# Performance work log

Measured on AMD Instinct MI355X. Metric: run time of the kernel, lower is better.

## Reference

```python
import jax, jax.numpy as jnp
import numpy as np
from jax import lax
from jax.scipy.special import logsumexp

B, T, K = 256, 1024, 64


def setup_inputs() -> dict:
    key = jax.random.key(0)
    k1, k2, k3 = jax.random.split(key, 3)
    y_true = jax.random.randint(k1, (B, T), 0, K)  # 0 == pad tag
    emissions = jax.random.normal(k2, (B, T, K), dtype=jnp.float32)
    transition = jax.random.normal(k3, (K, K), dtype=jnp.float32) * 0.1
    return {"y_true": y_true, "emissions": emissions, "transition": transition}


def _log_partition(emissions, mask, transition):
    # alpha_0 = emissions[:, 0, :] (TF code does not mask step 0)
    alpha0 = emissions[:, 0, :]  # [B, K]

    def step(alpha, xs):
        emit_t, m_t = xs  # [B, K], [B]
        # score[b, i, j] = alpha[b, i] + transition[i, j] + emit_t[b, j]
        score = alpha[:, :, None] + transition[None, :, :] + emit_t[:, None, :]
        new_a = logsumexp(score, axis=1)  # [B, K]
        new_a = jnp.where(m_t[:, None] > 0, new_a, alpha)
        return new_a, None

    xs = (jnp.swapaxes(emissions[:, 1:, :], 0, 1),  # [T-1, B, K]
          jnp.swapaxes(mask[:, 1:], 0, 1))           # [T-1, B]
    alpha, _ = lax.scan(step, alpha0, xs)
    return logsumexp(alpha, axis=1)  # [B]


def reference(y_true, emissions, transition):
    mask = (y_true != 0).astype(emissions.dtype)  # [B, T]
    yt = y_true.astype(jnp.int32)

    # emission scores of the gold path on masked emissions
    em_masked = emissions * mask[:, :, None]
    e_scores = jnp.take_along_axis(em_masked, yt[:, :, None], axis=2)[..., 0].sum(axis=1)  # [B]

    # transition scores of the gold path
    prev, nxt = yt[:, :-1], yt[:, 1:]
    t_scores = (transition[prev, nxt] * mask[:, 1:]).sum(axis=1)  # [B]

    log_z = _log_partition(emissions, mask, transition)  # [B]
    ll = e_scores + t_scores - log_z
    return -jnp.mean(ll)
```

## Files before the change

kernel.cpp:

```cpp
#include <hip/hip_runtime.h>

#define LOG2E 1.44269504088896340736f
#define LN2   0.69314718055994530942f

typedef short bf4 __attribute__((ext_vector_type(4)));
typedef float f4  __attribute__((ext_vector_type(4)));

static __device__ __forceinline__ unsigned short f2bf_rne(float f) {
    unsigned u = __float_as_uint(f);
    u += 0x7FFFu + ((u >> 16) & 1u);
    return (unsigned short)(u >> 16);
}
static __device__ __forceinline__ unsigned pack_bf_trunc(float lo, float hi) {
    return __builtin_amdgcn_perm(__float_as_uint(hi), __float_as_uint(lo), 0x07060302u);
}

static __device__ __forceinline__ f4 mfma16(bf4 a, bf4 b, f4 c) {
#if __has_builtin(__builtin_amdgcn_mfma_f32_16x16x16bf16_1k)
    return __builtin_amdgcn_mfma_f32_16x16x16bf16_1k(a, b, c, 0, 0, 0);
#else
    f4 d;
    asm("v_mfma_f32_16x16x16_bf16 %0, %1, %2, %3" : "=v"(d) : "v"(a), "v"(b), "v"(c));
    return d;
#endif
}
static __device__ __forceinline__ void mfma_fence() {
#if !__has_builtin(__builtin_amdgcn_mfma_f32_16x16x16bf16_1k)
    asm volatile("s_nop 7\ns_nop 7");
#endif
}

__global__ __attribute__((amdgpu_flat_work_group_size(64, 64), amdgpu_waves_per_eu(4)))
void crf_scan(const int* __restrict__ yg, const float* __restrict__ em,
              const float* __restrict__ tr, unsigned short* __restrict__ Pg)
{
    constexpr int T = 1024;
    const int c = blockIdx.x, b = blockIdx.y;
    const int lane = threadIdx.x, nl = lane & 15, q = lane >> 4;

    __shared__ __align__(16) float d_sh[64];

    bf4 afr[4][4];
    #pragma unroll
    for (int mt = 0; mt < 4; ++mt)
        #pragma unroll
        for (int kt = 0; kt < 4; ++kt) {
            bf4 v;
            #pragma unroll
            for (int j = 0; j < 4; ++j) {
                const int k = 16 * kt + 4 * q + j, m = 16 * mt + nl;
                v[j] = (short)f2bf_rne(exp2f(tr[k * 64 + m] * LOG2E));
            }
            afr[mt][kt] = v;
        }

    bf4 bfr[4][4];
    #pragma unroll
    for (int kt = 0; kt < 4; ++kt)
        #pragma unroll
        for (int nt = 0; nt < 4; ++nt) {
            bf4 v;
            #pragma unroll
            for (int j = 0; j < 4; ++j)
                v[j] = (short)((kt == nt && nl == 4 * q + j) ? 0x3F80 : 0);
            bfr[kt][nt] = v;
        }

    const int t0 = 1 + 64 * c;
    const int nsteps = (c == 15) ? 63 : 64;
    const float* emb = em + (size_t)b * T * 64;

    int tl = t0 + lane; if (tl > T - 1) tl = T - 1;
    const int yvl = yg[b * T + tl];
    const unsigned long long msk = __ballot(lane < nsteps && yvl != 0);

    float ldc = emb[t0 * 64 + lane];
    for (int s = 0; s < nsteps; ++s) {
        int tn = t0 + s + 1; if (tn > T - 1) tn = T - 1;
        const float ldn = emb[tn * 64 + lane];
        if ((msk >> s) & 1ull) {
            d_sh[lane] = exp2f(ldc * LOG2E - 7.0f);
            f4 dq[4];
            #pragma unroll
            for (int mt = 0; mt < 4; ++mt)
                dq[mt] = *(const f4*)&d_sh[16 * mt + 4 * q];
            #pragma unroll
            for (int nt = 0; nt < 4; ++nt) {
                f4 acc[4];
                #pragma unroll
                for (int mt = 0; mt < 4; ++mt) {
                    f4 a = mfma16(afr[mt][0], bfr[0][nt], (f4)(0.0f));
                    a = mfma16(afr[mt][1], bfr[1][nt], a);
                    a = mfma16(afr[mt][2], bfr[2][nt], a);
                    a = mfma16(afr[mt][3], bfr[3][nt], a);
                    acc[mt] = a;
                }
                mfma_fence();
                #pragma unroll
                for (int mt = 0; mt < 4; ++mt) {
                    union { uint2 u; bf4 v2; } wv;
                    wv.u.x = pack_bf_trunc(acc[mt][0] * dq[mt][0], acc[mt][1] * dq[mt][1]);
                    wv.u.y = pack_bf_trunc(acc[mt][2] * dq[mt][2], acc[mt][3] * dq[mt][3]);
                    bfr[mt][nt] = wv.v2;
                }
            }
        }
        ldc = ldn;
    }

    unsigned short* pg = Pg + ((size_t)(b * 16 + c) << 12);
    #pragma unroll
    for (int nt = 0; nt < 4; ++nt)
        #pragma unroll
        for (int kt = 0; kt < 4; ++kt)
            *(uint2*)(pg + (16 * nt + nl) * 64 + 16 * kt + 4 * q) =
                *(const uint2*)&bfr[kt][nt];
}

__global__ __attribute__((amdgpu_flat_work_group_size(256, 256)))
void crf_combine(const int* __restrict__ yg, const float* __restrict__ em,
                 const float* __restrict__ tr, const unsigned short* __restrict__ Pg,
                 float* __restrict__ out)
{
    constexpr int T = 1024;
    const int b = blockIdx.x, tid = threadIdx.x;
    const int w = tid >> 6, j = tid & 63;

    __shared__ __align__(16) float v_sh[64];
    __shared__ float red[3][4];

    float ep = 0.f, tp = 0.f; int cnt = 0;
    float v = 0.f, L = 0.f, vs = 0.f;

    if (w == 0) {
        const float e0 = em[(size_t)b * T * 64 + j];
        float M0 = e0;
        #pragma unroll
        for (int o = 32; o > 0; o >>= 1) M0 = fmaxf(M0, __shfl_xor(M0, o, 64));
        v = exp2f((e0 - M0) * LOG2E);
        L = M0;

        const unsigned short* row = Pg + ((size_t)(b * 16) << 12) + j * 64;
        uint4 pA[8], pB[8];
        #pragma unroll
        for (int r = 0; r < 8; ++r) pA[r] = *(const uint4*)(row + r * 8);

#define CHUNK_STEP(CUR, NXT, CIDX)                                                 \
        do {                                                                       \
            if ((CIDX) + 1 < 16) {      \
                const unsigned short* rn = row + ((size_t)((CIDX) + 1) << 12);     \
                _Pragma("unroll")                                                  \
                for (int r = 0; r < 8; ++r) NXT[r] = *(const uint4*)(rn + r * 8);  \
            }                                                                      \
            v_sh[j] = v;                             \
            float s0 = 0.f, s1 = 0.f, s2 = 0.f, s3 = 0.f;                          \
            _Pragma("unroll")                                                      \
            for (int r = 0; r < 8; ++r) {                                          \
                const uint4 qq = CUR[r];                                           \
                const float* vp = &v_sh[r * 8];                                    \
                s0 = fmaf(__uint_as_float(qq.x << 16),         vp[0], s0);         \
                s1 = fmaf(__uint_as_float(qq.x & 0xFFFF0000u), vp[1], s1);         \
                s2 = fmaf(__uint_as_float(qq.y << 16),         vp[2], s2);         \
                s3 = fmaf(__uint_as_float(qq.y & 0xFFFF0000u), vp[3], s3);         \
                s0 = fmaf(__uint_as_float(qq.z << 16),         vp[4], s0);         \
                s1 = fmaf(__uint_as_float(qq.z & 0xFFFF0000u), vp[5], s1);         \
                s2 = fmaf(__uint_as_float(qq.w << 16),         vp[6], s2);         \
                s3 = fmaf(__uint_as_float(qq.w & 0xFFFF0000u), vp[7], s3);         \
            }                                                                      \
            float s = (s0 + s1) + (s2 + s3);                                       \
            const unsigned sb =                                                    \
                (unsigned)__builtin_amdgcn_readlane((int)__float_as_uint(s), 0);   \
            const int ef = (int)((sb >> 23) & 0xFF);                               \
            if (ef > 0 && ef < 255 && ef != 127) {       \
                const int E = ef - 127;                                            \
                s *= __uint_as_float((unsigned)(127 - E) << 23);                   \
                L += (float)E * LN2;                                               \
            }                                                                      \
            v = s;                                                                 \
        } while (0)

        for (int cc = 0; cc < 16; cc += 2) {
            CHUNK_STEP(pA, pB, cc);
            CHUNK_STEP(pB, pA, cc + 1);
        }
#undef CHUNK_STEP

        vs = v;
        #pragma unroll
        for (int o = 32; o > 0; o >>= 1) vs += __shfl_xor(vs, o, 64);
    } else {
        const int* yb = yg + b * T;
        const int wt = tid - 64;
        for (int t = 1 + wt; t < T; t += 192) {
            const int yt = yb[t];
            if (yt != 0) {
                ++cnt;
                tp += tr[yb[t - 1] * 64 + yt];
                ep += em[((size_t)b * T + t) * 64 + yt];
            }
        }
        if (tid == 64) {
            const int y0 = yb[0];
            if (y0 != 0) ep += em[(size_t)b * T * 64 + y0];
        }
        #pragma unroll
        for (int o = 32; o > 0; o >>= 1) {
            ep  += __shfl_xor(ep, o, 64);
            tp  += __shfl_xor(tp, o, 64);
            cnt += __shfl_xor(cnt, o, 64);
        }
        if (j == 0) { red[0][w] = ep; red[1][w] = tp; red[2][w] = (float)cnt; }
    }
    __syncthreads();

    if (tid == 0) {
        const float eps = red[0][1] + red[0][2] + red[0][3];
        const float tps = red[1][1] + red[1][2] + red[1][3];
        const float cs  = red[2][1] + red[2][2] + red[2][3];
        const float logz = L + 7.0f * LN2 * cs + __log2f(vs) * LN2;
        atomicAdd(out, (eps + tps - logz) * (-1.0f / 256.0f));
    }
}

extern "C" void kernel_launch(void* const* d_in, const int* in_sizes, int n_in,
                              void* d_out, int out_size, void* d_ws, size_t ws_size,
                              hipStream_t stream) {
    const int*   y  = (const int*)d_in[0];
    const float* em = (const float*)d_in[1];
    const float* tr = (const float*)d_in[2];
    float* out = (float*)d_out;
    unsigned short* Pg = (unsigned short*)d_ws;

    hipMemsetAsync(out, 0, sizeof(float), stream);
    crf_scan<<<dim3(16, 256), dim3(64), 0, stream>>>(y, em, tr, Pg);
    crf_combine<<<dim3(256), dim3(256), 0, stream>>>(y, em, tr, Pg, out);
}
```

Baseline: 246.2 us.

## Interleave two independent chunk chains per wave in the CRF scan kernel

Each wavefront now processes two time chunks (c and c+8) of the same sequence, interleaving their MFMA chains so one chain's latency can hide behind the other. Masked steps are handled by a branchless select instead of skipping, so both chains always run the full MFMA work. The grid is halved and register pressure roughly doubles for the B-state fragments, which may reduce occupancy. The waves_per_eu hint is relaxed to allow that.

```diff
diff --git a/kernel.cpp b/kernel.cpp
--- a/kernel.cpp
+++ b/kernel.cpp
@@ -30,15 +30,15 @@
 #endif
 }
 
-__global__ __attribute__((amdgpu_flat_work_group_size(64, 64), amdgpu_waves_per_eu(4)))
+__global__ __attribute__((amdgpu_flat_work_group_size(64, 64), amdgpu_waves_per_eu(2, 4)))
 void crf_scan(const int* __restrict__ yg, const float* __restrict__ em,
               const float* __restrict__ tr, unsigned short* __restrict__ Pg)
 {
     constexpr int T = 1024;
-    const int c = blockIdx.x, b = blockIdx.y;
+    const int cA = blockIdx.x, b = blockIdx.y, cB = cA + 8;
     const int lane = threadIdx.x, nl = lane & 15, q = lane >> 4;
 
-    __shared__ __align__(16) float d_sh[64];
+    __shared__ __align__(16) float d_sh[2][64];
 
     bf4 afr[4][4];
     #pragma unroll
@@ -54,7 +54,7 @@
             afr[mt][kt] = v;
         }
 
-    bf4 bfr[4][4];
+    bf4 bfrA[4][4], bfrB[4][4];
     #pragma unroll
     for (int kt = 0; kt < 4; ++kt)
         #pragma unroll
@@ -63,58 +63,82 @@
             #pragma unroll
             for (int j = 0; j < 4; ++j)
                 v[j] = (short)((kt == nt && nl == 4 * q + j) ? 0x3F80 : 0);
-            bfr[kt][nt] = v;
-        }
-
-    const int t0 = 1 + 64 * c;
-    const int nsteps = (c == 15) ? 63 : 64;
+            bfrA[kt][nt] = v;
+            bfrB[kt][nt] = v;
+        }
+
     const float* emb = em + (size_t)b * T * 64;
-
-    int tl = t0 + lane; if (tl > T - 1) tl = T - 1;
-    const int yvl = yg[b * T + tl];
-    const unsigned long long msk = __ballot(lane < nsteps && yvl != 0);
-
-    float ldc = emb[t0 * 64 + lane];
-    for (int s = 0; s < nsteps; ++s) {
-        int tn = t0 + s + 1; if (tn > T - 1) tn = T - 1;
-        const float ldn = emb[tn * 64 + lane];
-        if ((msk >> s) & 1ull) {
-            d_sh[lane] = exp2f(ldc * LOG2E - 7.0f);
-            f4 dq[4];
-            #pragma unroll
-            for (int mt = 0; mt < 4; ++mt)
-                dq[mt] = *(const f4*)&d_sh[16 * mt + 4 * q];
-            #pragma unroll
-            for (int nt = 0; nt < 4; ++nt) {
-                f4 acc[4];
-                #pragma unroll
-                for (int mt = 0; mt < 4; ++mt) {
-                    f4 a = mfma16(afr[mt][0], bfr[0][nt], (f4)(0.0f));
-                    a = mfma16(afr[mt][1], bfr[1][nt], a);
-                    a = mfma16(afr[mt][2], bfr[2][nt], a);
-                    a = mfma16(afr[mt][3], bfr[3][nt], a);
-                    acc[mt] = a;
-                }
-                mfma_fence();
-                #pragma unroll
-                for (int mt = 0; mt < 4; ++mt) {
-                    union { uint2 u; bf4 v2; } wv;
-                    wv.u.x = pack_bf_trunc(acc[mt][0] * dq[mt][0], acc[mt][1] * dq[mt][1]);
-                    wv.u.y = pack_bf_trunc(acc[mt][2] * dq[mt][2], acc[mt][3] * dq[mt][3]);
-                    bfr[mt][nt] = wv.v2;
-                }
-            }
-        }
-        ldc = ldn;
+    const int t0A = 1 + 64 * cA;
+    const int t0B = 1 + 64 * cB;
+    const int nsB = (cB == 15) ? 63 : 64;
+
+    const unsigned long long mskA = __ballot(yg[b * T + t0A + lane] != 0);
+    int tlB = t0B + lane; if (tlB > T - 1) tlB = T - 1;
+    const unsigned long long mskB = __ballot(lane < nsB && yg[b * T + tlB] != 0);
+
+    float ldA = emb[t0A * 64 + lane];
+    float ldB = emb[t0B * 64 + lane];
+
+    auto step = [&](bf4 (&bfr)[4][4], const f4 (&dq)[4], bool act) {
+        #pragma unroll
+        for (int nt = 0; nt < 4; ++nt) {
+            f4 acc[4];
+            #pragma unroll
+            for (int mt = 0; mt < 4; ++mt) {
+                f4 a = mfma16(afr[mt][0], bfr[0][nt], (f4)(0.0f));
+                a = mfma16(afr[mt][1], bfr[1][nt], a);
+                a = mfma16(afr[mt][2], bfr[2][nt], a);
+                a = mfma16(afr[mt][3], bfr[3][nt], a);
+                acc[mt] = a;
+            }
+            mfma_fence();
+            #pragma unroll
+            for (int mt = 0; mt < 4; ++mt) {
+                union { uint2 u; bf4 v2; } wv, od;
+                od.v2 = bfr[mt][nt];
+                wv.u.x = pack_bf_trunc(acc[mt][0] * dq[mt][0], acc[mt][1] * dq[mt][1]);
+                wv.u.y = pack_bf_trunc(acc[mt][2] * dq[mt][2], acc[mt][3] * dq[mt][3]);
+                wv.u.x = act ? wv.u.x : od.u.x;
+                wv.u.y = act ? wv.u.y : od.u.y;
+                bfr[mt][nt] = wv.v2;
+            }
+        }
+    };
+
+    for (int s = 0; s < 64; ++s) {
+        const int tnA = t0A + s + 1;
+        int tnB = t0B + s + 1; if (tnB > T - 1) tnB = T - 1;
+        const float lnA = emb[tnA * 64 + lane];
+        const float lnB = emb[tnB * 64 + lane];
+
+        d_sh[0][lane] = exp2f(ldA * LOG2E - 7.0f);
+        d_sh[1][lane] = exp2f(ldB * LOG2E - 7.0f);
+        f4 dqA[4], dqB[4];
+        #pragma unroll
+        for (int mt = 0; mt < 4; ++mt) {
+            dqA[mt] = *(const f4*)&d_sh[0][16 * mt + 4 * q];
+            dqB[mt] = *(const f4*)&d_sh[1][16 * mt + 4 * q];
+        }
+
+        const bool aA = (mskA >> s) & 1ull;
+        const bool aB = (mskB >> s) & 1ull;
+        step(bfrA, dqA, aA);
+        step(bfrB, dqB, aB);
+
+        ldA = lnA; ldB = lnB;
     }
 
-    unsigned short* pg = Pg + ((size_t)(b * 16 + c) << 12);
+    unsigned short* pgA = Pg + ((size_t)(b * 16 + cA) << 12);
+    unsigned short* pgB = Pg + ((size_t)(b * 16 + cB) << 12);
     #pragma unroll
     for (int nt = 0; nt < 4; ++nt)
         #pragma unroll
-        for (int kt = 0; kt < 4; ++kt)
-            *(uint2*)(pg + (16 * nt + nl) * 64 + 16 * kt + 4 * q) =
-                *(const uint2*)&bfr[kt][nt];
+        for (int kt = 0; kt < 4; ++kt) {
+            *(uint2*)(pgA + (16 * nt + nl) * 64 + 16 * kt + 4 * q) =
+                *(const uint2*)&bfrA[kt][nt];
+            *(uint2*)(pgB + (16 * nt + nl) * 64 + 16 * kt + 4 * q) =
+                *(const uint2*)&bfrB[kt][nt];
+        }
 }
 
 __global__ __attribute__((amdgpu_flat_work_group_size(256, 256)))
@@ -232,6 +256,6 @@
     unsigned short* Pg = (unsigned short*)d_ws;
 
     hipMemsetAsync(out, 0, sizeof(float), stream);
-    crf_scan<<<dim3(16, 256), dim3(64), 0, stream>>>(y, em, tr, Pg);
+    crf_scan<<<dim3(8, 256), dim3(64), 0, stream>>>(y, em, tr, Pg);
     crf_combine<<<dim3(256), dim3(256), 0, stream>>>(y, em, tr, Pg, out);
 }
```

Result: slower. 256.6 us (+4.2%).

## Switch scan matmuls to 16x16x32 bf16 MFMA with permuted row layout

Applied to the files above, without the earlier changes.

Replaces the 16x16x16 bf16 MFMA chain (4 per output tile) with the gfx950 16x16x32 bf16 instruction (2 per tile). It permutes the transition rows so each output tile's accumulators pack directly into the next step's 8-wide B operand. This halves the MFMA issue count on the serial per-step dependency chain. The occupancy hint is also relaxed to waves_per_eu(2,4), which can change register allocation.

```diff
diff --git a/kernel.cpp b/kernel.cpp
--- a/kernel.cpp
+++ b/kernel.cpp
@@ -3,7 +3,7 @@
 #define LOG2E 1.44269504088896340736f
 #define LN2   0.69314718055994530942f
 
-typedef short bf4 __attribute__((ext_vector_type(4)));
+typedef short bf8 __attribute__((ext_vector_type(8)));
 typedef float f4  __attribute__((ext_vector_type(4)));
 
 static __device__ __forceinline__ unsigned short f2bf_rne(float f) {
@@ -15,22 +15,7 @@
     return __builtin_amdgcn_perm(__float_as_uint(hi), __float_as_uint(lo), 0x07060302u);
 }
 
-static __device__ __forceinline__ f4 mfma16(bf4 a, bf4 b, f4 c) {
-#if __has_builtin(__builtin_amdgcn_mfma_f32_16x16x16bf16_1k)
-    return __builtin_amdgcn_mfma_f32_16x16x16bf16_1k(a, b, c, 0, 0, 0);
-#else
-    f4 d;
-    asm("v_mfma_f32_16x16x16_bf16 %0, %1, %2, %3" : "=v"(d) : "v"(a), "v"(b), "v"(c));
-    return d;
-#endif
-}
-static __device__ __forceinline__ void mfma_fence() {
-#if !__has_builtin(__builtin_amdgcn_mfma_f32_16x16x16bf16_1k)
-    asm volatile("s_nop 7\ns_nop 7");
-#endif
-}
-
-__global__ __attribute__((amdgpu_flat_work_group_size(64, 64), amdgpu_waves_per_eu(4)))
+__global__ __attribute__((amdgpu_flat_work_group_size(64, 64), amdgpu_waves_per_eu(2, 4)))
 void crf_scan(const int* __restrict__ yg, const float* __restrict__ em,
               const float* __restrict__ tr, unsigned short* __restrict__ Pg)
 {
@@ -40,29 +25,31 @@
 
     __shared__ __align__(16) float d_sh[64];
 
-    bf4 afr[4][4];
+    bf8 afr[4][2];
     #pragma unroll
-    for (int mt = 0; mt < 4; ++mt)
-        #pragma unroll
-        for (int kt = 0; kt < 4; ++kt) {
-            bf4 v;
-            #pragma unroll
-            for (int j = 0; j < 4; ++j) {
-                const int k = 16 * kt + 4 * q + j, m = 16 * mt + nl;
-                v[j] = (short)f2bf_rne(exp2f(tr[k * 64 + m] * LOG2E));
+    for (int mt = 0; mt < 4; ++mt) {
+        const int g = 32 * (mt >> 1) + 8 * (nl >> 2) + 4 * (mt & 1) + (nl & 3);
+        #pragma unroll
+        for (int ka = 0; ka < 2; ++ka) {
+            bf8 v;
+            #pragma unroll
+            for (int j = 0; j < 8; ++j) {
+                const int k = 32 * ka + 8 * q + j;
+                v[j] = (short)f2bf_rne(exp2f(tr[k * 64 + g] * LOG2E));
             }
-            afr[mt][kt] = v;
-        }
-
-    bf4 bfr[4][4];
+            afr[mt][ka] = v;
+        }
+    }
+
+    bf8 bfr[2][4];
     #pragma unroll
-    for (int kt = 0; kt < 4; ++kt)
+    for (int kt = 0; kt < 2; ++kt)
         #pragma unroll
         for (int nt = 0; nt < 4; ++nt) {
-            bf4 v;
-            #pragma unroll
-            for (int j = 0; j < 4; ++j)
-                v[j] = (short)((kt == nt && nl == 4 * q + j) ? 0x3F80 : 0);
+            bf8 v;
+            #pragma unroll
+            for (int j = 0; j < 8; ++j)
+                v[j] = (short)((32 * kt + 8 * q + j == 16 * nt + nl) ? 0x3F80 : 0);
             bfr[kt][nt] = v;
         }
 
@@ -83,25 +70,29 @@
             f4 dq[4];
             #pragma unroll
             for (int mt = 0; mt < 4; ++mt)
-                dq[mt] = *(const f4*)&d_sh[16 * mt + 4 * q];
+                dq[mt] = *(const f4*)&d_sh[32 * (mt >> 1) + 4 * (mt & 1) + 8 * q];
             #pragma unroll
             for (int nt = 0; nt < 4; ++nt) {
                 f4 acc[4];
                 #pragma unroll
                 for (int mt = 0; mt < 4; ++mt) {
-                    f4 a = mfma16(afr[mt][0], bfr[0][nt], (f4)(0.0f));
-                    a = mfma16(afr[mt][1], bfr[1][nt], a);
-                    a = mfma16(afr[mt][2], bfr[2][nt], a);
-                    a = mfma16(afr[mt][3], bfr[3][nt], a);
-                    acc[mt] = a;
+                    f4 a = __builtin_amdgcn_mfma_f32_16x16x32_bf16(
+                               afr[mt][0], bfr[0][nt], (f4)(0.0f), 0, 0, 0);
+                    acc[mt] = __builtin_amdgcn_mfma_f32_16x16x32_bf16(
+                               afr[mt][1], bfr[1][nt], a, 0, 0, 0);
                 }
-                mfma_fence();
                 #pragma unroll
-                for (int mt = 0; mt < 4; ++mt) {
-                    union { uint2 u; bf4 v2; } wv;
-                    wv.u.x = pack_bf_trunc(acc[mt][0] * dq[mt][0], acc[mt][1] * dq[mt][1]);
-                    wv.u.y = pack_bf_trunc(acc[mt][2] * dq[mt][2], acc[mt][3] * dq[mt][3]);
-                    bfr[mt][nt] = wv.v2;
+                for (int kt = 0; kt < 2; ++kt) {
+                    union { uint4 u; bf8 v8; } wv;
+                    wv.u.x = pack_bf_trunc(acc[2*kt  ][0] * dq[2*kt  ][0],
+                                           acc[2*kt  ][1] * dq[2*kt  ][1]);
+                    wv.u.y = pack_bf_trunc(acc[2*kt  ][2] * dq[2*kt  ][2],
+                                           acc[2*kt  ][3] * dq[2*kt  ][3]);
+                    wv.u.z = pack_bf_trunc(acc[2*kt+1][0] * dq[2*kt+1][0],
+                                           acc[2*kt+1][1] * dq[2*kt+1][1]);
+                    wv.u.w = pack_bf_trunc(acc[2*kt+1][2] * dq[2*kt+1][2],
+                                           acc[2*kt+1][3] * dq[2*kt+1][3]);
+                    bfr[kt][nt] = wv.v8;
                 }
             }
         }
@@ -112,9 +103,9 @@
     #pragma unroll
     for (int nt = 0; nt < 4; ++nt)
         #pragma unroll
-        for (int kt = 0; kt < 4; ++kt)
-            *(uint2*)(pg + (16 * nt + nl) * 64 + 16 * kt + 4 * q) =
-                *(const uint2*)&bfr[kt][nt];
+        for (int kt = 0; kt < 2; ++kt)
+            *(uint4*)(pg + (16 * nt + nl) * 64 + 32 * kt + 8 * q) =
+                *(const uint4*)&bfr[kt][nt];
 }
 
 __global__ __attribute__((amdgpu_flat_work_group_size(256, 256)))
```

Result: faster. 203.4 us (-17.4%).
